# Performance work log

Measured on AMD Instinct MI355X. Metric: run time of the kernel, lower is better.

The kernel has to match this reference:

```python
import jax, jax.numpy as jnp
import numpy as np

VOCAB = 91557
WORD_DIM = 512
HIDDEN = 1024
B, T = 256, 128


def lstm_maxpool(x_emb, W_ih, W_hh, b_ih, b_hh):
    """x_emb: [B, T, D]. PyTorch LSTMCell recurrence (zero init state),
    then elementwise max over time of the hidden states."""
    Bq = x_emb.shape[0]
    H = W_hh.shape[1]

    def step(carry, x_t):
        h, c = carry
        gates = x_t @ W_ih.T + b_ih + h @ W_hh.T + b_hh  # [B, 4H]
        i, f, g, o = jnp.split(gates, 4, axis=-1)  # PyTorch gate order i,f,g,o
        i = jax.nn.sigmoid(i)
        f = jax.nn.sigmoid(f)
        g = jnp.tanh(g)
        o = jax.nn.sigmoid(o)
        c = f * c + i * g
        h = o * jnp.tanh(c)
        return (h, c), h

    h0 = jnp.zeros((Bq, H), x_emb.dtype)
    (_h, _c), hs = jax.lax.scan(step, (h0, h0), jnp.swapaxes(x_emb, 0, 1))  # hs: [T, B, H]
    return jnp.max(hs, axis=0)  # [B, H]


def setup_inputs() -> dict:
    key = jax.random.key(0)
    ks = jax.random.split(key, 9)
    question = jax.random.randint(ks[0], (B, T), 0, VOCAB)
    sentence = jax.random.randint(ks[1], (B, T), 0, VOCAB)
    emb = jax.random.normal(ks[2], (VOCAB, WORD_DIM), dtype=jnp.float32) * 0.02
    W_ih = jax.random.normal(ks[3], (4 * HIDDEN, WORD_DIM), dtype=jnp.float32) * 0.02
    W_hh = jax.random.normal(ks[4], (4 * HIDDEN, HIDDEN), dtype=jnp.float32) * 0.02
    b_ih = jax.random.normal(ks[5], (4 * HIDDEN,), dtype=jnp.float32) * 0.02
    b_hh = jax.random.normal(ks[6], (4 * HIDDEN,), dtype=jnp.float32) * 0.02
    W_last = jax.random.normal(ks[7], (2, 2 * HIDDEN), dtype=jnp.float32) * 0.02
    b_last = jax.random.normal(ks[8], (2,), dtype=jnp.float32) * 0.02
    return {
        "question": question, "sentence": sentence,
        "emb": emb, "W_ih": W_ih, "W_hh": W_hh, "b_ih": b_ih, "b_hh": b_hh,
        "W_last": W_last, "b_last": b_last,
    }


def reference(question, sentence, emb, W_ih, W_hh, b_ih, b_hh, W_last, b_last):
    q_embedded = emb[question]  # [B, T, D]
    s_embedded = emb[sentence]  # [B, T, D]
    hq = lstm_maxpool(q_embedded, W_ih, W_hh, b_ih, b_hh)  # [B, H]
    hs = lstm_maxpool(s_embedded, W_ih, W_hh, b_ih, b_hh)  # [B, H]
    out = jnp.concatenate([hq, hs], axis=1) @ W_last.T + b_last  # [B, 2]
    return jax.nn.sigmoid(out)
```

## Files before the change

kernel.cpp:

```cpp
#include <hip/hip_runtime.h>
#include <hip/hip_bf16.h>
#include <cstdint>


typedef __bf16 bf16x8 __attribute__((ext_vector_type(8)));
typedef float f32x4 __attribute__((ext_vector_type(4)));

__device__ __forceinline__ float sigm(float x) {
    return 1.0f / (1.0f + __expf(-x));
}
__device__ __forceinline__ float tanh_fast(float x) {
    x = fminf(15.0f, fmaxf(-15.0f, x));
    float e = __expf(2.0f * x);
    return (e - 1.0f) / (e + 1.0f);
}
__device__ __forceinline__ ushort f2bu(float f) {
    __hip_bfloat16 h = __float2bfloat16(f);
    return __builtin_bit_cast(unsigned short, h);
}
__device__ __forceinline__ float bu2f(ushort u) {
    return __uint_as_float(((unsigned)u) << 16);
}
__device__ __forceinline__ void gl_lds16(const void* g, void* l) {
    __builtin_amdgcn_global_load_lds(
        (const __attribute__((address_space(1))) unsigned int*)g,
        (__attribute__((address_space(3))) unsigned int*)l, 16, 0, 0);
}

__global__ void prep_weights(const float* __restrict__ Wih,
                             const float* __restrict__ Whh,
                             const float* __restrict__ bih,
                             const float* __restrict__ bhh,
                             __hip_bfloat16* __restrict__ WcT,
                             float* __restrict__ biasc) {
    int p = blockIdx.y;
    int k = blockIdx.x * blockDim.x + threadIdx.x;
    int r = (p & 3) * 1024 + (p >> 2);
    float v = (k < 512) ? Wih[(size_t)r * 512 + k]
                        : Whh[(size_t)r * 1024 + (k - 512)];
    WcT[(size_t)p * 1536 + k] = __float2bfloat16(v);
    if (k == 0) biasc[p] = bih[r] + bhh[r];
}

__global__ void gather_embed(const int* __restrict__ q,
                             const int* __restrict__ s,
                             const float* __restrict__ emb,
                             ushort* __restrict__ X) {
    int rb = blockIdx.x;
    int t = rb >> 9;
    int b = rb & 511;
    int tok = (b < 256) ? q[b * 128 + t] : s[(b - 256) * 128 + t];
    const float2* src = (const float2*)(emb + (size_t)tok * 512);
    ushort2* dst = (ushort2*)(X + (size_t)rb * 512);
    float2 v = src[threadIdx.x];
    ushort2 o;
    o.x = f2bu(v.x);
    o.y = f2bu(v.y);
    dst[threadIdx.x] = o;
}

__global__ void init_state(float* __restrict__ C, float* __restrict__ HMAX,
                           ushort* __restrict__ H0) {
    int i = blockIdx.x * 256 + threadIdx.x;
    C[i] = 0.0f;
    HMAX[i] = -1e30f;
    H0[i] = 0;
}

__global__ __launch_bounds__(256, 2) void xproj_gemm(
    const ushort* __restrict__ X,
    const ushort* __restrict__ WcT,
    ushort* __restrict__ Xb,
    int row0) {
    __shared__ __align__(16) ushort As[128 * 128];
    __shared__ __align__(16) ushort Bs[128 * 128];

    const int tid = threadIdx.x;
    const int n0 = blockIdx.x * 128;
    const int m0 = blockIdx.y * 128;
    const int lane = tid & 63;
    const int w = tid >> 6;
    const int quad = lane >> 4;
    const int l16 = lane & 15;
    const int wm = (w >> 1) * 64;
    const int wn = (w & 1) * 64;

    f32x4 acc[4][4] = {};

    for (int it = 0; it < 4; ++it) {
        const int k0 = it * 128;
        __syncthreads();
#pragma unroll
        for (int i = 0; i < 8; ++i) {
            int u = i * 256 + tid;
            int r = u >> 4;
            int cs = (u & 15) ^ (r & 15);
            gl_lds16(X + (size_t)(row0 + m0 + r) * 512 + k0 + cs * 8,
                     (ushort*)As + (size_t)u * 8);
            gl_lds16(WcT + (size_t)(n0 + r) * 1536 + k0 + cs * 8,
                     (ushort*)Bs + (size_t)u * 8);
        }
        __syncthreads();
#pragma unroll
        for (int kb = 0; kb < 4; ++kb) {
            bf16x8 af[4], bfr[4];
            const int vsel = (kb << 2) | quad;
#pragma unroll
            for (int mi = 0; mi < 4; ++mi)
                af[mi] = *(const bf16x8*)(As +
                    (((wm + mi * 16 + l16) << 4) + (vsel ^ l16)) * 8);
#pragma unroll
            for (int ni = 0; ni < 4; ++ni)
                bfr[ni] = *(const bf16x8*)(Bs +
                    (((wn + ni * 16 + l16) << 4) + (vsel ^ l16)) * 8);
#pragma unroll
            for (int mi = 0; mi < 4; ++mi)
#pragma unroll
                for (int ni = 0; ni < 4; ++ni)
                    acc[mi][ni] = __builtin_amdgcn_mfma_f32_16x16x32_bf16(
                        af[mi], bfr[ni], acc[mi][ni], 0, 0, 0);
        }
    }

#pragma unroll
    for (int mi = 0; mi < 4; ++mi)
#pragma unroll
        for (int ni = 0; ni < 4; ++ni)
#pragma unroll
            for (int rg = 0; rg < 4; ++rg)
                Xb[(size_t)(m0 + wm + mi * 16 + quad * 4 + rg) * 4096 +
                   (n0 + wn + ni * 16 + l16)] = f2bu(acc[mi][ni][rg]);
}

__global__ __launch_bounds__(256, 2) void lstm_step(
    const ushort* __restrict__ Xb,
    const ushort* __restrict__ WcT,
    const float* __restrict__ biasc,
    const ushort* __restrict__ Hin,
    ushort* __restrict__ Hout,
    float* __restrict__ C,
    float* __restrict__ HMAX,
    int t) {
    __shared__ __align__(16) ushort As[64 * 128];
    __shared__ __align__(16) ushort Bs[128 * 128];
    __shared__ float Gs[64][132];
    __shared__ float biasS[128];

    const int tid = threadIdx.x;
    const int n0 = blockIdx.x * 128;
    const int m0 = blockIdx.y * 64;

    if (tid < 128) biasS[tid] = biasc[n0 + tid];

    const int lane = tid & 63;
    const int w = tid >> 6;
    const int quad = lane >> 4;
    const int l16 = lane & 15;
    const int wm = (w >> 1) * 32;
    const int wn = (w & 1) * 64;

    f32x4 acc[2][4] = {};

    for (int it = 0; it < 8; ++it) {
        const int k0 = it * 128;
        __syncthreads();
#pragma unroll
        for (int i = 0; i < 4; ++i) {
            int u = i * 256 + tid;
            int r = u >> 4;
            int cs = (u & 15) ^ (r & 15);
            gl_lds16(Hin + (size_t)(m0 + r) * 1024 + k0 + cs * 8,
                     (ushort*)As + (size_t)u * 8);
        }
#pragma unroll
        for (int i = 0; i < 8; ++i) {
            int u = i * 256 + tid;
            int r = u >> 4;
            int cs = (u & 15) ^ (r & 15);
            gl_lds16(WcT + (size_t)(n0 + r) * 1536 + 512 + k0 + cs * 8,
                     (ushort*)Bs + (size_t)u * 8);
        }
        __syncthreads();
#pragma unroll
        for (int kb = 0; kb < 4; ++kb) {
            bf16x8 af[2], bfr[4];
            const int vsel = (kb << 2) | quad;
#pragma unroll
            for (int mi = 0; mi < 2; ++mi)
                af[mi] = *(const bf16x8*)(As +
                    (((wm + mi * 16 + l16) << 4) + (vsel ^ l16)) * 8);
#pragma unroll
            for (int ni = 0; ni < 4; ++ni)
                bfr[ni] = *(const bf16x8*)(Bs +
                    (((wn + ni * 16 + l16) << 4) + (vsel ^ l16)) * 8);
#pragma unroll
            for (int mi = 0; mi < 2; ++mi)
#pragma unroll
                for (int ni = 0; ni < 4; ++ni)
                    acc[mi][ni] = __builtin_amdgcn_mfma_f32_16x16x32_bf16(
                        af[mi], bfr[ni], acc[mi][ni], 0, 0, 0);
        }
    }

#pragma unroll
    for (int mi = 0; mi < 2; ++mi)
#pragma unroll
        for (int ni = 0; ni < 4; ++ni)
#pragma unroll
            for (int rg = 0; rg < 4; ++rg)
                Gs[wm + mi * 16 + quad * 4 + rg][wn + ni * 16 + l16] =
                    acc[mi][ni][rg];
    __syncthreads();

    const int m = tid >> 2;
    const int c4 = tid & 3;
    const int col0 = c4 * 32;
    const size_t hrow = (size_t)(m0 + m) * 1024;
    const int j0 = (n0 >> 2) + c4 * 8;
    const ushort* xp =
        Xb + (size_t)((t & 7) * 512 + m0 + m) * 4096 + n0 + col0;

    f32x4 cold0 = *(const f32x4*)&C[hrow + j0];
    f32x4 cold1 = *(const f32x4*)&C[hrow + j0 + 4];
    f32x4 hm0 = *(const f32x4*)&HMAX[hrow + j0];
    f32x4 hm1 = *(const f32x4*)&HMAX[hrow + j0 + 4];
    f32x4 cn0, cn1;
    ushort4 hb0, hb1;
#pragma unroll
    for (int u = 0; u < 8; ++u) {
        int cb = col0 + 4 * u;
        float gi = Gs[m][cb + 0] + bu2f(xp[4 * u + 0]) + biasS[cb + 0];
        float gf = Gs[m][cb + 1] + bu2f(xp[4 * u + 1]) + biasS[cb + 1];
        float gg = Gs[m][cb + 2] + bu2f(xp[4 * u + 2]) + biasS[cb + 2];
        float go = Gs[m][cb + 3] + bu2f(xp[4 * u + 3]) + biasS[cb + 3];
        float iv = sigm(gi);
        float fv = sigm(gf);
        float gv = tanh_fast(gg);
        float ov = sigm(go);
        float cold = (u < 4) ? cold0[u & 3] : cold1[u & 3];
        float cn = fv * cold + iv * gv;
        float h = ov * tanh_fast(cn);
        ushort hbits = f2bu(h);
        if (u < 4) {
            cn0[u & 3] = cn;
            hm0[u & 3] = fmaxf(hm0[u & 3], h);
            ((ushort*)&hb0)[u & 3] = hbits;
        } else {
            cn1[u & 3] = cn;
            hm1[u & 3] = fmaxf(hm1[u & 3], h);
            ((ushort*)&hb1)[u & 3] = hbits;
        }
    }
    *(f32x4*)&C[hrow + j0] = cn0;
    *(f32x4*)&C[hrow + j0 + 4] = cn1;
    *(f32x4*)&HMAX[hrow + j0] = hm0;
    *(f32x4*)&HMAX[hrow + j0 + 4] = hm1;
    *(ushort4*)&Hout[hrow + j0] = hb0;
    *(ushort4*)&Hout[hrow + j0 + 4] = hb1;
}

__global__ void final_out(const float* __restrict__ HMAX,
                          const float* __restrict__ Wl,
                          const float* __restrict__ bl,
                          float* __restrict__ out) {
    int b = blockIdx.x;
    int tid = threadIdx.x;
    float s0 = 0.0f, s1 = 0.0f;
    for (int j = tid; j < 1024; j += 256) {
        float hq = HMAX[(size_t)b * 1024 + j];
        float hs = HMAX[(size_t)(256 + b) * 1024 + j];
        s0 += hq * Wl[j] + hs * Wl[1024 + j];
        s1 += hq * Wl[2048 + j] + hs * Wl[3072 + j];
    }
    __shared__ float r0[256], r1[256];
    r0[tid] = s0;
    r1[tid] = s1;
    __syncthreads();
    for (int off = 128; off > 0; off >>= 1) {
        if (tid < off) {
            r0[tid] += r0[tid + off];
            r1[tid] += r1[tid + off];
        }
        __syncthreads();
    }
    if (tid == 0) {
        out[b * 2 + 0] = sigm(r0[0] + bl[0]);
        out[b * 2 + 1] = sigm(r1[0] + bl[1]);
    }
}

extern "C" void kernel_launch(void* const* d_in, const int* in_sizes, int n_in,
                              void* d_out, int out_size, void* d_ws,
                              size_t ws_size, hipStream_t stream) {
    const int* q = (const int*)d_in[0];
    const int* s = (const int*)d_in[1];
    const float* emb = (const float*)d_in[2];
    const float* Wih = (const float*)d_in[3];
    const float* Whh = (const float*)d_in[4];
    const float* bih = (const float*)d_in[5];
    const float* bhh = (const float*)d_in[6];
    const float* Wl = (const float*)d_in[7];
    const float* bl = (const float*)d_in[8];
    float* out = (float*)d_out;

    char* ws = (char*)d_ws;
    __hip_bfloat16* WcT = (__hip_bfloat16*)(ws + 0);
    float* biasc = (float*)(ws + 12582912);
    ushort* X = (ushort*)(ws + 12599296);
    ushort* Xb = (ushort*)(ws + 79708160);
    ushort* H0 = (ushort*)(ws + 113262592);
    ushort* H1 = (ushort*)(ws + 114311168);
    float* C = (float*)(ws + 115359744);
    float* HMAX = (float*)(ws + 117456896);

    prep_weights<<<dim3(6, 4096), 256, 0, stream>>>(Wih, Whh, bih, bhh, WcT,
                                                    biasc);
    gather_embed<<<65536, 256, 0, stream>>>(q, s, emb, X);
    init_state<<<2048, 256, 0, stream>>>(C, HMAX, H0);

    ushort* hin = H0;
    ushort* hout = H1;
    for (int c = 0; c < 16; ++c) {
        xproj_gemm<<<dim3(32, 32), 256, 0, stream>>>(X, (const ushort*)WcT, Xb,
                                                     c * 4096);
        for (int tt = 0; tt < 8; ++tt) {
            int t = c * 8 + tt;
            lstm_step<<<dim3(32, 8), 256, 0, stream>>>(
                Xb, (const ushort*)WcT, biasc, hin, hout, C, HMAX, t);
            ushort* tmp = hin;
            hin = hout;
            hout = tmp;
        }
    }
    final_out<<<256, 256, 0, stream>>>(HMAX, Wl, bl, out);
}
```

Before: 2.496 ms.

## Fuse eight LSTM steps into persistent kernel with weight-stationary LDS and group barriers

Replaces 128 per-timestep lstm_step launches with 16 lstm_chunk launches. Each block keeps its 64-column slice of W_hh resident in LDS across 8 timesteps and carries c and the running max in registers, synchronising with the other blocks of its row group through an atomic-counter spin barrier. Weight rows are permuted so each block owns whole gate quadruples, the bias is folded into the input-projection GEMM, and the embedding gather is done per chunk into a smaller buffer. This removes launch overhead and the repeated W_hh reloads, but it relies on all 256 blocks being co-resident for the spin barrier to avoid deadlock.

```diff
diff --git a/kernel.cpp b/kernel.cpp
--- a/kernel.cpp
+++ b/kernel.cpp
@@ -35,43 +35,46 @@
                              float* __restrict__ biasc) {
     int p = blockIdx.y;
     int k = blockIdx.x * blockDim.x + threadIdx.x;
-    int r = (p & 3) * 1024 + (p >> 2);
+    int nb = p >> 6;
+    int g = (p >> 4) & 3;
+    int jl = p & 15;
+    int r = g * 1024 + nb * 16 + jl;
     float v = (k < 512) ? Wih[(size_t)r * 512 + k]
                         : Whh[(size_t)r * 1024 + (k - 512)];
     WcT[(size_t)p * 1536 + k] = __float2bfloat16(v);
     if (k == 0) biasc[p] = bih[r] + bhh[r];
 }
 
-__global__ void gather_embed(const int* __restrict__ q,
+__global__ void gather_chunk(const int* __restrict__ q,
                              const int* __restrict__ s,
                              const float* __restrict__ emb,
-                             ushort* __restrict__ X) {
-    int rb = blockIdx.x;
-    int t = rb >> 9;
-    int b = rb & 511;
+                             ushort* __restrict__ Xc, int t0) {
+    int rr = blockIdx.x;
+    int t = t0 + (rr >> 9);
+    int b = rr & 511;
     int tok = (b < 256) ? q[b * 128 + t] : s[(b - 256) * 128 + t];
     const float2* src = (const float2*)(emb + (size_t)tok * 512);
-    ushort2* dst = (ushort2*)(X + (size_t)rb * 512);
     float2 v = src[threadIdx.x];
     ushort2 o;
     o.x = f2bu(v.x);
     o.y = f2bu(v.y);
-    dst[threadIdx.x] = o;
+    ((ushort2*)(Xc + (size_t)rr * 512))[threadIdx.x] = o;
 }
 
 __global__ void init_state(float* __restrict__ C, float* __restrict__ HMAX,
-                           ushort* __restrict__ H0) {
+                           ushort* __restrict__ H0, int* __restrict__ cnt) {
     int i = blockIdx.x * 256 + threadIdx.x;
     C[i] = 0.0f;
     HMAX[i] = -1e30f;
     H0[i] = 0;
+    if (i < 64) cnt[i] = 0;
 }
 
 __global__ __launch_bounds__(256, 2) void xproj_gemm(
-    const ushort* __restrict__ X,
+    const ushort* __restrict__ Xc,
     const ushort* __restrict__ WcT,
-    ushort* __restrict__ Xb,
-    int row0) {
+    const float* __restrict__ biasc,
+    ushort* __restrict__ Xb) {
     __shared__ __align__(16) ushort As[128 * 128];
     __shared__ __align__(16) ushort Bs[128 * 128];
 
@@ -95,7 +98,7 @@
             int u = i * 256 + tid;
             int r = u >> 4;
             int cs = (u & 15) ^ (r & 15);
-            gl_lds16(X + (size_t)(row0 + m0 + r) * 512 + k0 + cs * 8,
+            gl_lds16(Xc + (size_t)(m0 + r) * 512 + k0 + cs * 8,
                      (ushort*)As + (size_t)u * 8);
             gl_lds16(WcT + (size_t)(n0 + r) * 1536 + k0 + cs * 8,
                      (ushort*)Bs + (size_t)u * 8);
@@ -125,138 +128,158 @@
 #pragma unroll
     for (int mi = 0; mi < 4; ++mi)
 #pragma unroll
-        for (int ni = 0; ni < 4; ++ni)
+        for (int ni = 0; ni < 4; ++ni) {
+            float bv = biasc[n0 + wn + ni * 16 + l16];
 #pragma unroll
             for (int rg = 0; rg < 4; ++rg)
                 Xb[(size_t)(m0 + wm + mi * 16 + quad * 4 + rg) * 4096 +
-                   (n0 + wn + ni * 16 + l16)] = f2bu(acc[mi][ni][rg]);
-}
-
-__global__ __launch_bounds__(256, 2) void lstm_step(
+                   (n0 + wn + ni * 16 + l16)] = f2bu(acc[mi][ni][rg] + bv);
+        }
+}
+
+__global__ __launch_bounds__(256, 1) void lstm_chunk(
     const ushort* __restrict__ Xb,
     const ushort* __restrict__ WcT,
-    const float* __restrict__ biasc,
-    const ushort* __restrict__ Hin,
-    ushort* __restrict__ Hout,
+    ushort* __restrict__ Hbuf,
     float* __restrict__ C,
     float* __restrict__ HMAX,
-    int t) {
-    __shared__ __align__(16) ushort As[64 * 128];
-    __shared__ __align__(16) ushort Bs[128 * 128];
-    __shared__ float Gs[64][132];
-    __shared__ float biasS[128];
+    int* __restrict__ bcnt,
+    int t0, int tgt0) {
+    __shared__ ushort Ws[64][1032];
 
     const int tid = threadIdx.x;
-    const int n0 = blockIdx.x * 128;
-    const int m0 = blockIdx.y * 64;
-
-    if (tid < 128) biasS[tid] = biasc[n0 + tid];
-
+    const int b = blockIdx.x;
+    const int mg = (b & 7) >> 1;
+    const int nb = ((b >> 3) << 1) | (b & 1);
+    const int m0 = mg * 128;
+    const int n0 = nb * 64;
+    const int jb = nb * 16;
+    const int w = tid >> 6;
     const int lane = tid & 63;
-    const int w = tid >> 6;
     const int quad = lane >> 4;
     const int l16 = lane & 15;
-    const int wm = (w >> 1) * 32;
-    const int wn = (w & 1) * 64;
-
-    f32x4 acc[2][4] = {};
-
-    for (int it = 0; it < 8; ++it) {
-        const int k0 = it * 128;
-        __syncthreads();
-#pragma unroll
-        for (int i = 0; i < 4; ++i) {
-            int u = i * 256 + tid;
-            int r = u >> 4;
-            int cs = (u & 15) ^ (r & 15);
-            gl_lds16(Hin + (size_t)(m0 + r) * 1024 + k0 + cs * 8,
-                     (ushort*)As + (size_t)u * 8);
-        }
-#pragma unroll
-        for (int i = 0; i < 8; ++i) {
-            int u = i * 256 + tid;
-            int r = u >> 4;
-            int cs = (u & 15) ^ (r & 15);
-            gl_lds16(WcT + (size_t)(n0 + r) * 1536 + 512 + k0 + cs * 8,
-                     (ushort*)Bs + (size_t)u * 8);
-        }
-        __syncthreads();
-#pragma unroll
-        for (int kb = 0; kb < 4; ++kb) {
-            bf16x8 af[2], bfr[4];
-            const int vsel = (kb << 2) | quad;
-#pragma unroll
-            for (int mi = 0; mi < 2; ++mi)
-                af[mi] = *(const bf16x8*)(As +
-                    (((wm + mi * 16 + l16) << 4) + (vsel ^ l16)) * 8);
+
+#pragma unroll 4
+    for (int i = 0; i < 32; ++i) {
+        int u = i * 256 + tid;
+        int c = u >> 7;
+        int kc = u & 127;
+        uint4 v = *(const uint4*)(WcT + (size_t)(n0 + c) * 1536 + 512 + kc * 8);
+        *(uint4*)&Ws[c][kc * 8] = v;
+    }
+
+    float creg[8], hmx[8];
+    const int rbase = m0 + w * 32 + quad * 4;
+#pragma unroll
+    for (int idx = 0; idx < 8; ++idx) {
+        int row = rbase + (idx >> 2) * 16 + (idx & 3);
+        creg[idx] = C[(size_t)row * 1024 + jb + l16];
+        hmx[idx] = HMAX[(size_t)row * 1024 + jb + l16];
+    }
+    __syncthreads();
+
+#pragma unroll 1
+    for (int st = 0; st < 8; ++st) {
+        const int t = t0 + st;
+        const ushort* Hin = Hbuf + ((size_t)(t & 1) << 19);
+        ushort* Hout = Hbuf + ((size_t)((t + 1) & 1) << 19);
+
+        ushort xbv[8][4];
+        const ushort* xbase =
+            Xb + (size_t)(st * 512 + rbase) * 4096 + n0 + l16;
+#pragma unroll
+        for (int idx = 0; idx < 8; ++idx) {
+            const ushort* xr =
+                xbase + (size_t)((idx >> 2) * 16 + (idx & 3)) * 4096;
+#pragma unroll
+            for (int g = 0; g < 4; ++g) xbv[idx][g] = xr[g * 16];
+        }
+
+        f32x4 acc[2][4] = {};
+        const ushort* arow0 =
+            Hin + (size_t)(m0 + w * 32 + l16) * 1024 + quad * 8;
+        const ushort* arow1 = arow0 + 16 * 1024;
+
+        bf16x8 apf[8][2];
+        bf16x8 bpf[4][4];
+#pragma unroll
+        for (int s = 0; s < 8; ++s) {
+            apf[s][0] = *(const bf16x8*)(arow0 + s * 32);
+            apf[s][1] = *(const bf16x8*)(arow1 + s * 32);
+        }
+#pragma unroll
+        for (int s = 0; s < 4; ++s)
 #pragma unroll
             for (int ni = 0; ni < 4; ++ni)
-                bfr[ni] = *(const bf16x8*)(Bs +
-                    (((wn + ni * 16 + l16) << 4) + (vsel ^ l16)) * 8);
-#pragma unroll
-            for (int mi = 0; mi < 2; ++mi)
+                bpf[s][ni] =
+                    *(const bf16x8*)&Ws[ni * 16 + l16][s * 32 + quad * 8];
+
+#pragma unroll
+        for (int s = 0; s < 32; ++s) {
+            bf16x8 a0 = apf[s & 7][0];
+            bf16x8 a1 = apf[s & 7][1];
+            bf16x8 b0 = bpf[s & 3][0];
+            bf16x8 b1 = bpf[s & 3][1];
+            bf16x8 b2 = bpf[s & 3][2];
+            bf16x8 b3 = bpf[s & 3][3];
+            if (s + 8 < 32) {
+                apf[s & 7][0] = *(const bf16x8*)(arow0 + (s + 8) * 32);
+                apf[s & 7][1] = *(const bf16x8*)(arow1 + (s + 8) * 32);
+            }
+            if (s + 4 < 32) {
 #pragma unroll
                 for (int ni = 0; ni < 4; ++ni)
-                    acc[mi][ni] = __builtin_amdgcn_mfma_f32_16x16x32_bf16(
-                        af[mi], bfr[ni], acc[mi][ni], 0, 0, 0);
-        }
-    }
-
-#pragma unroll
-    for (int mi = 0; mi < 2; ++mi)
-#pragma unroll
-        for (int ni = 0; ni < 4; ++ni)
-#pragma unroll
-            for (int rg = 0; rg < 4; ++rg)
-                Gs[wm + mi * 16 + quad * 4 + rg][wn + ni * 16 + l16] =
-                    acc[mi][ni][rg];
-    __syncthreads();
-
-    const int m = tid >> 2;
-    const int c4 = tid & 3;
-    const int col0 = c4 * 32;
-    const size_t hrow = (size_t)(m0 + m) * 1024;
-    const int j0 = (n0 >> 2) + c4 * 8;
-    const ushort* xp =
-        Xb + (size_t)((t & 7) * 512 + m0 + m) * 4096 + n0 + col0;
-
-    f32x4 cold0 = *(const f32x4*)&C[hrow + j0];
-    f32x4 cold1 = *(const f32x4*)&C[hrow + j0 + 4];
-    f32x4 hm0 = *(const f32x4*)&HMAX[hrow + j0];
-    f32x4 hm1 = *(const f32x4*)&HMAX[hrow + j0 + 4];
-    f32x4 cn0, cn1;
-    ushort4 hb0, hb1;
-#pragma unroll
-    for (int u = 0; u < 8; ++u) {
-        int cb = col0 + 4 * u;
-        float gi = Gs[m][cb + 0] + bu2f(xp[4 * u + 0]) + biasS[cb + 0];
-        float gf = Gs[m][cb + 1] + bu2f(xp[4 * u + 1]) + biasS[cb + 1];
-        float gg = Gs[m][cb + 2] + bu2f(xp[4 * u + 2]) + biasS[cb + 2];
-        float go = Gs[m][cb + 3] + bu2f(xp[4 * u + 3]) + biasS[cb + 3];
-        float iv = sigm(gi);
-        float fv = sigm(gf);
-        float gv = tanh_fast(gg);
-        float ov = sigm(go);
-        float cold = (u < 4) ? cold0[u & 3] : cold1[u & 3];
-        float cn = fv * cold + iv * gv;
-        float h = ov * tanh_fast(cn);
-        ushort hbits = f2bu(h);
-        if (u < 4) {
-            cn0[u & 3] = cn;
-            hm0[u & 3] = fmaxf(hm0[u & 3], h);
-            ((ushort*)&hb0)[u & 3] = hbits;
-        } else {
-            cn1[u & 3] = cn;
-            hm1[u & 3] = fmaxf(hm1[u & 3], h);
-            ((ushort*)&hb1)[u & 3] = hbits;
-        }
-    }
-    *(f32x4*)&C[hrow + j0] = cn0;
-    *(f32x4*)&C[hrow + j0 + 4] = cn1;
-    *(f32x4*)&HMAX[hrow + j0] = hm0;
-    *(f32x4*)&HMAX[hrow + j0 + 4] = hm1;
-    *(ushort4*)&Hout[hrow + j0] = hb0;
-    *(ushort4*)&Hout[hrow + j0 + 4] = hb1;
+                    bpf[s & 3][ni] = *(const bf16x8*)&Ws[ni * 16 + l16]
+                                                       [(s + 4) * 32 + quad * 8];
+            }
+            acc[0][0] = __builtin_amdgcn_mfma_f32_16x16x32_bf16(a0, b0, acc[0][0], 0, 0, 0);
+            acc[0][1] = __builtin_amdgcn_mfma_f32_16x16x32_bf16(a0, b1, acc[0][1], 0, 0, 0);
+            acc[0][2] = __builtin_amdgcn_mfma_f32_16x16x32_bf16(a0, b2, acc[0][2], 0, 0, 0);
+            acc[0][3] = __builtin_amdgcn_mfma_f32_16x16x32_bf16(a0, b3, acc[0][3], 0, 0, 0);
+            acc[1][0] = __builtin_amdgcn_mfma_f32_16x16x32_bf16(a1, b0, acc[1][0], 0, 0, 0);
+            acc[1][1] = __builtin_amdgcn_mfma_f32_16x16x32_bf16(a1, b1, acc[1][1], 0, 0, 0);
+            acc[1][2] = __builtin_amdgcn_mfma_f32_16x16x32_bf16(a1, b2, acc[1][2], 0, 0, 0);
+            acc[1][3] = __builtin_amdgcn_mfma_f32_16x16x32_bf16(a1, b3, acc[1][3], 0, 0, 0);
+        }
+
+#pragma unroll
+        for (int idx = 0; idx < 8; ++idx) {
+            const int mi = idx >> 2;
+            const int rg = idx & 3;
+            float gi = acc[mi][0][rg] + bu2f(xbv[idx][0]);
+            float gf = acc[mi][1][rg] + bu2f(xbv[idx][1]);
+            float gg = acc[mi][2][rg] + bu2f(xbv[idx][2]);
+            float go = acc[mi][3][rg] + bu2f(xbv[idx][3]);
+            float cn = sigm(gf) * creg[idx] + sigm(gi) * tanh_fast(gg);
+            float h = sigm(go) * tanh_fast(cn);
+            creg[idx] = cn;
+            hmx[idx] = fmaxf(hmx[idx], h);
+            int row = rbase + mi * 16 + rg;
+            Hout[(size_t)row * 1024 + jb + l16] = f2bu(h);
+        }
+
+        if (st < 7) {
+            __threadfence();
+            __syncthreads();
+            if (tid == 0) {
+                atomicAdd(&bcnt[mg], 1);
+                const int target = tgt0 + 64 * (st + 1);
+                while (__hip_atomic_load(&bcnt[mg], __ATOMIC_RELAXED,
+                                         __HIP_MEMORY_SCOPE_AGENT) < target) {
+                    __builtin_amdgcn_s_sleep(2);
+                }
+            }
+            __syncthreads();
+            __threadfence();
+        }
+    }
+
+#pragma unroll
+    for (int idx = 0; idx < 8; ++idx) {
+        int row = rbase + (idx >> 2) * 16 + (idx & 3);
+        C[(size_t)row * 1024 + jb + l16] = creg[idx];
+        HMAX[(size_t)row * 1024 + jb + l16] = hmx[idx];
+    }
 }
 
 __global__ void final_out(const float* __restrict__ HMAX,
@@ -306,31 +329,24 @@
     char* ws = (char*)d_ws;
     __hip_bfloat16* WcT = (__hip_bfloat16*)(ws + 0);
     float* biasc = (float*)(ws + 12582912);
-    ushort* X = (ushort*)(ws + 12599296);
-    ushort* Xb = (ushort*)(ws + 79708160);
-    ushort* H0 = (ushort*)(ws + 113262592);
-    ushort* H1 = (ushort*)(ws + 114311168);
-    float* C = (float*)(ws + 115359744);
-    float* HMAX = (float*)(ws + 117456896);
+    ushort* Xc = (ushort*)(ws + 12599296);
+    ushort* Xb = (ushort*)(ws + 16793600);
+    ushort* Hbuf = (ushort*)(ws + 50348032);
+    float* C = (float*)(ws + 52445184);
+    float* HMAX = (float*)(ws + 54542336);
+    int* counters = (int*)(ws + 56639488);
 
     prep_weights<<<dim3(6, 4096), 256, 0, stream>>>(Wih, Whh, bih, bhh, WcT,
                                                     biasc);
-    gather_embed<<<65536, 256, 0, stream>>>(q, s, emb, X);
-    init_state<<<2048, 256, 0, stream>>>(C, HMAX, H0);
-
-    ushort* hin = H0;
-    ushort* hout = H1;
+    init_state<<<2048, 256, 0, stream>>>(C, HMAX, Hbuf, counters);
+
     for (int c = 0; c < 16; ++c) {
-        xproj_gemm<<<dim3(32, 32), 256, 0, stream>>>(X, (const ushort*)WcT, Xb,
-                                                     c * 4096);
-        for (int tt = 0; tt < 8; ++tt) {
-            int t = c * 8 + tt;
-            lstm_step<<<dim3(32, 8), 256, 0, stream>>>(
-                Xb, (const ushort*)WcT, biasc, hin, hout, C, HMAX, t);
-            ushort* tmp = hin;
-            hin = hout;
-            hout = tmp;
-        }
+        gather_chunk<<<4096, 256, 0, stream>>>(q, s, emb, Xc, c * 8);
+        xproj_gemm<<<dim3(32, 32), 256, 0, stream>>>(Xc, (const ushort*)WcT,
+                                                     biasc, Xb);
+        lstm_chunk<<<256, 256, 0, stream>>>(Xb, (const ushort*)WcT, Hbuf, C,
+                                            HMAX, counters, c * 8,
+                                            c * 7 * 64);
     }
     final_out<<<256, 256, 0, stream>>>(HMAX, Wl, bl, out);
 }
```

Result: slower. 7.163 ms (+186.9%).
